# Kernel optimization log

Hardware: AMD Instinct MI355X
Metric: run time of the kernel (lower is better)

## Reference

```python
import jax, jax.numpy as jnp
import numpy as np

B, C, H, W = 512, 64, 32, 64
NUM_NODE = 128


def setup_inputs() -> dict:
    key = jax.random.key(0)
    ks = jax.random.split(key, 11)
    f = jnp.float32
    def nrm(k, shape, s):
        return jax.random.normal(k, shape, f) * s
    return {
        "x":   jax.random.normal(ks[0], (B, C, H, W), f),
        "w11": nrm(ks[1], (32, 64, 1, 1), 0.1), "b11": nrm(ks[2], (32,), 0.05),
        "w12": nrm(ks[3], (16, 32, 3, 3), 0.1), "b12": nrm(ks[4], (16,), 0.05),
        "w21": nrm(ks[5], (8, 16, 1, 1), 0.1),  "b21": nrm(ks[6], (8,), 0.05),
        "w22": nrm(ks[7], (4, 8, 3, 3), 0.1),   "b22": nrm(ks[8], (4,), 0.05),
        "fcw": nrm(ks[9], (2 * NUM_NODE, 32 * 64 * 4), 0.05),
        "fcb": nrm(ks[10], (2 * NUM_NODE,), 0.05),
    }


def _conv_relu(x, w, b, pad):
    y = jax.lax.conv_general_dilated(
        x, w, window_strides=(1, 1), padding=[(pad, pad), (pad, pad)],
        dimension_numbers=("NCHW", "OIHW", "NCHW"))
    return jax.nn.relu(y + b[None, :, None, None])


def reference(x, w11, b11, w12, b12, w21, b21, w22, b22, fcw, fcb):
    # --- GraphGen3: conv stack -> fc -> n_Sigmoid -> [B, N, 2] ---
    h = _conv_relu(x, w11, b11, 0)
    h = _conv_relu(h, w12, b12, 1)
    h = _conv_relu(h, w21, b21, 0)
    h = _conv_relu(h, w22, b22, 1)          # [B, 4, 32, 64]
    z = h.reshape(h.shape[0], -1) @ fcw.T + fcb  # [B, 2N]
    c01 = jax.nn.sigmoid(3.0 * z).reshape(x.shape[0], -1, 2)  # n_Sigmoid(x, 3)
    # --- get_coord: scale normalized coords to pixel range ---
    Hd, Wd = x.shape[2], x.shape[3]
    coord = c01 * jnp.array([Hd - 1, Wd - 1], x.dtype)  # [B, N, 2]
    # --- th_batch_map_coordinates: clamp, corner gather, bilinear lerp ---
    ch = jnp.clip(coord[..., 0], 0.0, Hd - 1)
    cw = jnp.clip(coord[..., 1], 0.0, Wd - 1)
    h0 = jnp.floor(ch).astype(jnp.int32); h1 = jnp.ceil(ch).astype(jnp.int32)
    w0 = jnp.floor(cw).astype(jnp.int32); w1 = jnp.ceil(cw).astype(jnp.int32)
    bidx = jnp.arange(x.shape[0])[:, None]  # [B, 1]
    def gv(hi, wi):
        return x[bidx, :, hi, wi]           # gather -> [B, N, C]
    v_lt = gv(h0, w0); v_rt = gv(h1, w0)
    v_lb = gv(h0, w1); v_rb = gv(h1, w1)
    oh = (ch - h0.astype(x.dtype))[..., None]
    ow = (cw - w0.astype(x.dtype))[..., None]
    vt = v_lt + oh * (v_rt - v_lt)
    vb = v_lb + oh * (v_rb - v_lb)
    graph_feat = vt + ow * (vb - vt)        # [B, N, C] (matches permute(0,2,1))
    return graph_feat, coord
```

## Files before the change

### kernel.cpp

```cpp
#include <hip/hip_runtime.h>
#include <hip/hip_fp16.h>
#include <cstdint>

#define BATCH 512
#define CIN   64
#define HH    32
#define WW    64
#define HW    2048
#define C1    32
#define C2    16
#define C3    8
#define C4    4
#define NOUT  256
#define KFC   8192
#define NODES 128
#define KS    16
#define GF_SIZE (BATCH * NODES * CIN)

typedef __attribute__((ext_vector_type(8))) short bfrag;
typedef __attribute__((ext_vector_type(4))) float ffrag;

__device__ __forceinline__ ushort bf_trunc(float f) { return (ushort)(__float_as_uint(f) >> 16); }
__device__ __forceinline__ float  bf_truncf(float f) { return __uint_as_float(__float_as_uint(f) & 0xffff0000u); }
__device__ __forceinline__ ushort f2bf(float f) {
  uint32_t u = __float_as_uint(f);
  return (ushort)((u + 0x7fffu + ((u >> 16) & 1u)) >> 16);
}
__device__ __forceinline__ uint32_t pack2(float a, float b) {
  return (uint32_t)f2bf(a) | ((uint32_t)f2bf(b) << 16);
}
__device__ __forceinline__ uint32_t packhi2(float a, float b) {
  return (uint32_t)bf_trunc(a) | ((uint32_t)bf_trunc(b) << 16);
}
__device__ __forceinline__ ushort f2h(float f) { return __half_as_ushort(__float2half_rn(f)); }
__device__ __forceinline__ uint32_t packh2(float a, float b) {
  return (uint32_t)f2h(a) | ((uint32_t)f2h(b) << 16);
}
__device__ __forceinline__ float h2f(uint32_t u) { return __half2float(__ushort_as_half((ushort)u)); }
__device__ __forceinline__ float bf2f(ushort u) { return __uint_as_float(((uint32_t)u) << 16); }

__device__ __forceinline__ bfrag ld_frag4(const uint32_t* tp) {
  union { uint32_t u[4]; bfrag b; } c;
  c.u[0] = tp[0]; c.u[1] = tp[1]; c.u[2] = tp[2]; c.u[3] = tp[3];
  return c.b;
}

__global__ __launch_bounds__(256) void k_front(
    const float* __restrict__ x, const float* __restrict__ w11, const float* __restrict__ b11,
    const float* __restrict__ fcw, ushort* __restrict__ fcwh, ushort* __restrict__ fcwl,
    ushort* __restrict__ xt, ushort* __restrict__ h1g)
{
  if (blockIdx.y >= BATCH) {
    const int chunk = (blockIdx.y - BATCH) * 8 + blockIdx.x;
    const int i = (chunk * 256 + threadIdx.x) * 8;
    const float4 a = *(const float4*)(fcw + i);
    const float4 b = *(const float4*)(fcw + i + 4);
    uint4 hv, lv;
    hv.x = packhi2(a.x, a.y); hv.y = packhi2(a.z, a.w);
    hv.z = packhi2(b.x, b.y); hv.w = packhi2(b.z, b.w);
    lv.x = pack2(a.x - bf_truncf(a.x), a.y - bf_truncf(a.y));
    lv.y = pack2(a.z - bf_truncf(a.z), a.w - bf_truncf(a.w));
    lv.z = pack2(b.x - bf_truncf(b.x), b.y - bf_truncf(b.y));
    lv.w = pack2(b.z - bf_truncf(b.z), b.w - bf_truncf(b.w));
    *(uint4*)(fcwh + i) = hv;
    *(uint4*)(fcwl + i) = lv;
    return;
  }

  __shared__ uint32_t tb[256 * 33];
  const int t  = threadIdx.x;
  const int b  = blockIdx.y;
  const int rg = blockIdx.x;
  {
    const float* xp = x + (size_t)b * CIN * HW + rg * 256 + t;
    #pragma unroll
    for (int j = 0; j < 32; ++j) {
      float v0 = xp[(size_t)(2 * j) * HW];
      float v1 = xp[(size_t)(2 * j + 1) * HW];
      tb[t * 33 + j] = pack2(v0, v1);
    }
  }
  __syncthreads();

  {
    ushort* op = xt + ((size_t)b * HW + rg * 256) * CIN;
    #pragma unroll
    for (int k = 0; k < 8; ++k) {
      const int u = k * 256 + t;
      const int p = u >> 3, q = u & 7;
      uint4 v;
      v.x = tb[p * 33 + q * 4 + 0];
      v.y = tb[p * 33 + q * 4 + 1];
      v.z = tb[p * 33 + q * 4 + 2];
      v.w = tb[p * 33 + q * 4 + 3];
      *(uint4*)(op + (size_t)u * 8) = v;
    }
  }

  const int l  = t & 63;
  const int wv = t >> 6;
  const int lr = l & 15;
  const int lg = l >> 4;
  bfrag w1h[2][2], w1l[2][2];
  #pragma unroll
  for (int m = 0; m < 2; ++m) {
    #pragma unroll
    for (int ks = 0; ks < 2; ++ks) {
      const float* wp = w11 + (m * 16 + lr) * 64 + ks * 32 + lg * 8;
      #pragma unroll
      for (int e = 0; e < 8; ++e) {
        float v = wp[e];
        w1h[m][ks][e] = (short)bf_trunc(v);
        w1l[m][ks][e] = (short)f2bf(v - bf_truncf(v));
      }
    }
  }
  float bias1[2][4];
  #pragma unroll
  for (int m = 0; m < 2; ++m) {
    #pragma unroll
    for (int r = 0; r < 4; ++r) bias1[m][r] = b11[m * 16 + lg * 4 + r];
  }

  #pragma unroll
  for (int i = 0; i < 4; ++i) {
    const int pxl = (wv * 4 + i) * 16 + lr;
    const bfrag f0 = ld_frag4(&tb[pxl * 33 + lg * 4]);
    const bfrag f1 = ld_frag4(&tb[pxl * 33 + 16 + lg * 4]);
    ffrag a0 = {0.f, 0.f, 0.f, 0.f}, a1 = {0.f, 0.f, 0.f, 0.f};
    a0 = __builtin_amdgcn_mfma_f32_16x16x32_bf16(w1h[0][0], f0, a0, 0, 0, 0);
    a0 = __builtin_amdgcn_mfma_f32_16x16x32_bf16(w1l[0][0], f0, a0, 0, 0, 0);
    a0 = __builtin_amdgcn_mfma_f32_16x16x32_bf16(w1h[0][1], f1, a0, 0, 0, 0);
    a0 = __builtin_amdgcn_mfma_f32_16x16x32_bf16(w1l[0][1], f1, a0, 0, 0, 0);
    a1 = __builtin_amdgcn_mfma_f32_16x16x32_bf16(w1h[1][0], f0, a1, 0, 0, 0);
    a1 = __builtin_amdgcn_mfma_f32_16x16x32_bf16(w1l[1][0], f0, a1, 0, 0, 0);
    a1 = __builtin_amdgcn_mfma_f32_16x16x32_bf16(w1h[1][1], f1, a1, 0, 0, 0);
    a1 = __builtin_amdgcn_mfma_f32_16x16x32_bf16(w1l[1][1], f1, a1, 0, 0, 0);
    ushort* hp = h1g + ((size_t)b * HW + rg * 256 + pxl) * C1;
    #pragma unroll
    for (int m = 0; m < 2; ++m) {
      float v0 = fmaxf((m ? a1[0] : a0[0]) + bias1[m][0], 0.f);
      float v1 = fmaxf((m ? a1[1] : a0[1]) + bias1[m][1], 0.f);
      float v2 = fmaxf((m ? a1[2] : a0[2]) + bias1[m][2], 0.f);
      float v3 = fmaxf((m ? a1[3] : a0[3]) + bias1[m][3], 0.f);
      *(uint2*)(hp + m * 16 + lg * 4) = uint2{pack2(v0, v1), pack2(v2, v3)};
    }
  }
}

__global__ __launch_bounds__(256) void k_conv234(
    const ushort* __restrict__ h1g, const float* __restrict__ w12, const float* __restrict__ b12,
    const float* __restrict__ w21, const float* __restrict__ b21,
    const float* __restrict__ w22, const float* __restrict__ b22,
    ushort* __restrict__ h4, int b0)
{
  __shared__ __align__(16) char smem[12 * 66 * 64];
  const int tid = threadIdx.x;
  const int l   = tid & 63;
  const int wv  = tid >> 6;
  const int lr  = l & 15;
  const int lg  = l >> 4;
  const int r0  = blockIdx.x * 8;
  const int bg  = b0 + blockIdx.y;

  if (tid < 192) {
    int row = tid >> 4, half = (tid >> 3) & 1, q = tid & 7;
    int cell = row * 66 + (half ? 65 : 0);
    *(uint2*)(smem + (cell << 6) + q * 8) = uint2{0u, 0u};
  }

  {
    const int px = tid >> 2, q = tid & 3;
    const int colb  = px + 1;
    const int chunk = q ^ ((colb >> 1) & 3);
    #pragma unroll
    for (int ry = 0; ry < 12; ++ry) {
      const int y = r0 - 2 + ry;
      uint4 v = uint4{0u, 0u, 0u, 0u};
      if (y >= 0 && y < HH)
        v = *(const uint4*)(h1g + ((size_t)bg * HW + y * WW + px) * C1 + q * 8);
      *(uint4*)(smem + ((ry * 66 + colb) << 6) + (chunk << 4)) = v;
    }
  }
  __syncthreads();

  bfrag w2h[9], w2l[9];
  #pragma unroll
  for (int t = 0; t < 9; ++t) {
    const float* wp = w12 + lr * 288 + t;
    #pragma unroll
    for (int e = 0; e < 8; ++e) {
      float v = wp[(lg * 8 + e) * 9];
      w2h[t][e] = (short)bf_trunc(v);
      w2l[t][e] = (short)f2bf(v - bf_truncf(v));
    }
  }
  float bias2[4];
  #pragma unroll
  for (int r = 0; r < 4; ++r) bias2[r] = b12[lg * 4 + r];

  uint32_t ph0[10], ph1[10];
  #pragma unroll
  for (int i = 0; i < 10; ++i) {
    const int nt   = wv * 10 + i;
    const int hryo = nt >> 2;
    const int col0 = (nt & 3) << 4;
    ffrag acc = {0.f, 0.f, 0.f, 0.f};
    #pragma unroll
    for (int ky = 0; ky < 3; ++ky) {
      const int row = hryo + ky;
      #pragma unroll
      for (int kx = 0; kx < 3; ++kx) {
        const int colb  = col0 + lr + kx;
        const int chunk = lg ^ ((colb >> 1) & 3);
        const bfrag hv = *(const bfrag*)(smem + ((row * 66 + colb) << 6) + (chunk << 4));
        acc = __builtin_amdgcn_mfma_f32_16x16x32_bf16(w2h[ky * 3 + kx], hv, acc, 0, 0, 0);
        acc = __builtin_amdgcn_mfma_f32_16x16x32_bf16(w2l[ky * 3 + kx], hv, acc, 0, 0, 0);
      }
    }
    ph0[i] = packh2(fmaxf(acc[0] + bias2[0], 0.f), fmaxf(acc[1] + bias2[1], 0.f));
    ph1[i] = packh2(fmaxf(acc[2] + bias2[2], 0.f), fmaxf(acc[3] + bias2[3], 0.f));
  }
  __syncthreads();

  #pragma unroll
  for (int i = 0; i < 10; ++i) {
    const int nt   = wv * 10 + i;
    const int hryo = nt >> 2;
    const int col  = ((nt & 3) << 4) + lr;
    *(uint2*)(smem + ((hryo * 64 + col) << 5) + lg * 8) = uint2{ph0[i], ph1[i]};
  }
  __syncthreads();

  float* h3b = (float*)(smem + 20480);
  for (int p = tid; p < 640; p += 256) {
    const int ry = p >> 6, wc = p & 63;
    const int y  = r0 - 1 + ry;
    float* hd = h3b + (ry * 64 + wc) * 9;
    if (y >= 0 && y < HH) {
      const uint4 ua = *(const uint4*)(smem + ((ry * 64 + wc) << 5));
      const uint4 ub = *(const uint4*)(smem + ((ry * 64 + wc) << 5) + 16);
      uint32_t uw[8] = {ua.x, ua.y, ua.z, ua.w, ub.x, ub.y, ub.z, ub.w};
      float xv[16];
      #pragma unroll
      for (int j = 0; j < 8; ++j) {
        xv[2*j]   = h2f(uw[j] & 0xffffu);
        xv[2*j+1] = h2f(uw[j] >> 16);
      }
      float acc[C3];
      #pragma unroll
      for (int o = 0; o < C3; ++o) acc[o] = b21[o];
      #pragma unroll
      for (int c = 0; c < 16; ++c) {
        float v = xv[c];
        #pragma unroll
        for (int o = 0; o < C3; ++o)
          acc[o] = fmaf(v, w21[o * 16 + c], acc[o]);
      }
      #pragma unroll
      for (int c = 0; c < C3; ++c) hd[c] = fmaxf(acc[c], 0.f);
    } else {
      #pragma unroll
      for (int c = 0; c < C3; ++c) hd[c] = 0.f;
    }
  }
  __syncthreads();

  for (int p = tid; p < 512; p += 256) {
    const int yl = p >> 6, wc = p & 63, ry = yl + 1;
    float acc[C4] = {b22[0], b22[1], b22[2], b22[3]};
    #pragma unroll
    for (int ky = 0; ky < 3; ++ky) {
      #pragma unroll
      for (int kx = 0; kx < 3; ++kx) {
        const int wcc = wc + kx - 1;
        if (wcc < 0 || wcc >= WW) continue;
        const float* hb = h3b + ((ry + ky - 1) * 64 + wcc) * 9;
        const int tap = ky * 3 + kx;
        #pragma unroll
        for (int c = 0; c < C3; ++c) {
          float v = hb[c];
          #pragma unroll
          for (int o = 0; o < C4; ++o)
            acc[o] = fmaf(v, w22[(o * 8 + c) * 9 + tap], acc[o]);
        }
      }
    }
    const size_t base = (size_t)blockIdx.y * KFC + (r0 + yl) * WW + wc;
    #pragma unroll
    for (int o = 0; o < C4; ++o)
      h4[base + (size_t)o * HW] = f2bf(fmaxf(acc[o], 0.f));
  }
}

__global__ __launch_bounds__(256) void k_fc(
    const ushort* __restrict__ Ap_, const ushort* __restrict__ Bhp,
    const ushort* __restrict__ Blp, float* __restrict__ zpart, int cb)
{
  const int tid = threadIdx.x;
  const int l   = tid & 63;
  const int wv  = tid >> 6;
  const int lr  = l & 15;
  const int lg  = l >> 4;
  const int m0  = blockIdx.x * 64 + (wv >> 1) * 32;
  const int n0  = blockIdx.y * 64 + (wv & 1) * 32;
  const int k0  = blockIdx.z * (KFC / KS);

  int mrow[2], nrow[2];
  #pragma unroll
  for (int t = 0; t < 2; ++t) {
    int m = m0 + t * 16 + lr;
    mrow[t] = m < cb ? m : cb - 1;
    nrow[t] = n0 + t * 16 + lr;
  }
  ffrag acc[2][2] = {};

  #pragma unroll 1
  for (int kc = 0; kc < (KFC / KS) / 32; ++kc) {
    const int k = k0 + kc * 32 + lg * 8;
    bfrag ah[2], bh[2], bl[2];
    #pragma unroll
    for (int t = 0; t < 2; ++t) {
      ah[t] = *(const bfrag*)(Ap_ + (size_t)mrow[t] * KFC + k);
      bh[t] = *(const bfrag*)(Bhp + (size_t)nrow[t] * KFC + k);
      bl[t] = *(const bfrag*)(Blp + (size_t)nrow[t] * KFC + k);
    }
    #pragma unroll
    for (int mt = 0; mt < 2; ++mt) {
      #pragma unroll
      for (int nt = 0; nt < 2; ++nt) {
        acc[mt][nt] = __builtin_amdgcn_mfma_f32_16x16x32_bf16(ah[mt], bh[nt], acc[mt][nt], 0, 0, 0);
        acc[mt][nt] = __builtin_amdgcn_mfma_f32_16x16x32_bf16(ah[mt], bl[nt], acc[mt][nt], 0, 0, 0);
      }
    }
  }

  #pragma unroll
  for (int mt = 0; mt < 2; ++mt) {
    #pragma unroll
    for (int r = 0; r < 4; ++r) {
      const int m = m0 + mt * 16 + lg * 4 + r;
      if (m < cb) {
        #pragma unroll
        for (int nt = 0; nt < 2; ++nt)
          zpart[((size_t)blockIdx.z * cb + m) * NOUT + n0 + nt * 16 + lr] = acc[mt][nt][r];
      }
    }
  }
}

__global__ __launch_bounds__(256) void k_gather(
    const ushort* __restrict__ xt, const float* __restrict__ zpart,
    const float* __restrict__ fcb, float* __restrict__ out, int cb, int b0)
{
  const int bid = blockIdx.x;
  int bl, g;
  if ((cb & 7) == 0) {
    const int xcd = bid & 7;
    const int j   = bid >> 3;
    g  = j & 31;
    bl = (j >> 5) * 8 + xcd;
  } else {
    bl = bid >> 5;
    g  = bid & 31;
  }
  const int node = g * 4 + (threadIdx.x >> 6);
  const int l    = threadIdx.x & 63;
  const int bg   = b0 + bl;

  float val = 0.f;
  if (l < 2 * KS) {
    const int kb = l >> 1, comp = l & 1;
    val = zpart[((size_t)kb * cb + bl) * NOUT + node * 2 + comp];
  }
  #pragma unroll
  for (int off = 2; off < 2 * KS; off <<= 1) val += __shfl_xor(val, off);
  const float z0 = __shfl(val, 0) + fcb[node * 2 + 0];
  const float z1 = __shfl(val, 1) + fcb[node * 2 + 1];
  const float ch = 31.f / (1.f + __expf(-3.f * z0));
  const float cw = 63.f / (1.f + __expf(-3.f * z1));

  if (l < 2)
    out[GF_SIZE + (((size_t)bg * NODES + node) << 1) + l] = l ? cw : ch;

  const float chv = fminf(fmaxf(ch, 0.f), 31.f);
  const float cwv = fminf(fmaxf(cw, 0.f), 63.f);
  const float fh = floorf(chv), fw = floorf(cwv);
  const int h0 = (int)fh, h1i = (int)ceilf(chv);
  const int w0 = (int)fw, w1i = (int)ceilf(cwv);
  const float oh = chv - fh, ow = cwv - fw;
  const ushort* xbp = xt + (size_t)bg * HW * CIN + l;
  const float v_lt = bf2f(xbp[(size_t)(h0 * WW + w0) * CIN]);
  const float v_rt = bf2f(xbp[(size_t)(h1i * WW + w0) * CIN]);
  const float v_lb = bf2f(xbp[(size_t)(h0 * WW + w1i) * CIN]);
  const float v_rb = bf2f(xbp[(size_t)(h1i * WW + w1i) * CIN]);
  const float vt = v_lt + oh * (v_rt - v_lt);
  const float vb = v_lb + oh * (v_rb - v_lb);
  out[((size_t)bg * NODES + node) * CIN + l] = vt + ow * (vb - vt);
}

extern "C" void kernel_launch(void* const* d_in, const int* in_sizes, int n_in,
                              void* d_out, int out_size, void* d_ws, size_t ws_size,
                              hipStream_t stream)
{
  (void)in_sizes; (void)n_in; (void)out_size;
  const float* x   = (const float*)d_in[0];
  const float* w11 = (const float*)d_in[1];
  const float* b11 = (const float*)d_in[2];
  const float* w12 = (const float*)d_in[3];
  const float* b12 = (const float*)d_in[4];
  const float* w21 = (const float*)d_in[5];
  const float* b21 = (const float*)d_in[6];
  const float* w22 = (const float*)d_in[7];
  const float* b22 = (const float*)d_in[8];
  const float* fcw = (const float*)d_in[9];
  const float* fcb = (const float*)d_in[10];
  float* out = (float*)d_out;
  char* wsb  = (char*)d_ws;

  const size_t xtBytes = (size_t)BATCH * HW * CIN * 2;
  const size_t h1Bytes = (size_t)BATCH * HW * C1 * 2;
  const size_t perB    = 16384 + (size_t)KS * NOUT * 4;
  const size_t fixed   = xtBytes + h1Bytes + 2 * 4194304;
  size_t avail = ws_size > fixed ? ws_size - fixed : perB;
  size_t cbmax = avail / perB;
  int CB = (int)(cbmax < (size_t)BATCH ? cbmax : (size_t)BATCH);
  if (CB < 1) CB = 1;

  char* p = wsb;
  ushort* xtv  = (ushort*)p;  p += xtBytes;
  ushort* h1v  = (ushort*)p;  p += h1Bytes;
  ushort* h4v  = (ushort*)p;  p += (size_t)CB * 16384;
  float*  zpv  = (float*)p;   p += (size_t)CB * KS * NOUT * 4;
  ushort* fcwh = (ushort*)p;  p += 4194304;
  ushort* fcwl = (ushort*)p;

  k_front<<<dim3(8, BATCH + 128), 256, 0, stream>>>(x, w11, b11, fcw, fcwh, fcwl,
                                                    xtv, h1v);

  for (int b0 = 0; b0 < BATCH; b0 += CB) {
    const int cb = (BATCH - b0 < CB) ? (BATCH - b0) : CB;
    k_conv234<<<dim3(4, cb), 256, 0, stream>>>(h1v, w12, b12, w21, b21, w22, b22,
                                               h4v, b0);
    k_fc<<<dim3((cb + 63) / 64, 4, KS), 256, 0, stream>>>(h4v, fcwh, fcwl, zpv, cb);
    k_gather<<<dim3(cb * 32), 256, 0, stream>>>(xtv, zpv, fcb, out, cb, b0);
  }
}
```

Before: 212.6 us.

## Fuse all stages into one persistent cooperative kernel with grid syncs

Replaces the four separate launches (front, conv234, fc, gather) with a single persistent cooperative kernel that loops over tiles for each stage and separates stages with grid-wide syncs. The goal is to remove launch overhead and inter-kernel gaps. It also drops workspace-based batch chunking and assumes the workspace holds the full batch. In exchange, the persistent grid is limited by occupancy of a large fused kernel with 50KB shared memory, which may lower parallelism per stage, and grid syncs add their own cost.

```diff
diff --git a/kernel.cpp b/kernel.cpp
--- a/kernel.cpp
+++ b/kernel.cpp
@@ -1,6 +1,9 @@
 #include <hip/hip_runtime.h>
 #include <hip/hip_fp16.h>
+#include <hip/hip_cooperative_groups.h>
 #include <cstdint>
+
+namespace cg = cooperative_groups;
 
 #define BATCH 512
 #define CIN   64
@@ -43,6 +46,327 @@
   union { uint32_t u[4]; bfrag b; } c;
   c.u[0] = tp[0]; c.u[1] = tp[1]; c.u[2] = tp[2]; c.u[3] = tp[3];
   return c.b;
+}
+
+__global__ __launch_bounds__(256) void k_mega(
+    const float* __restrict__ x, const float* __restrict__ w11, const float* __restrict__ b11,
+    const float* __restrict__ w12, const float* __restrict__ b12,
+    const float* __restrict__ w21, const float* __restrict__ b21,
+    const float* __restrict__ w22, const float* __restrict__ b22,
+    const float* __restrict__ fcw, const float* __restrict__ fcb,
+    ushort* __restrict__ fcwh, ushort* __restrict__ fcwl,
+    ushort* __restrict__ xt, ushort* __restrict__ h1g, ushort* __restrict__ h4,
+    float* __restrict__ zpart, float* __restrict__ out)
+{
+  __shared__ __align__(16) char smem[50688];
+  cg::grid_group gg = cg::this_grid();
+  const int tid = threadIdx.x;
+  const int l   = tid & 63;
+  const int wv  = tid >> 6;
+  const int lr  = l & 15;
+  const int lg  = l >> 4;
+
+  {
+    bfrag w1h[2][2], w1l[2][2];
+    #pragma unroll
+    for (int m = 0; m < 2; ++m)
+      #pragma unroll
+      for (int ks = 0; ks < 2; ++ks) {
+        const float* wp = w11 + (m * 16 + lr) * 64 + ks * 32 + lg * 8;
+        #pragma unroll
+        for (int e = 0; e < 8; ++e) {
+          float v = wp[e];
+          w1h[m][ks][e] = (short)bf_trunc(v);
+          w1l[m][ks][e] = (short)f2bf(v - bf_truncf(v));
+        }
+      }
+    float bias1[2][4];
+    #pragma unroll
+    for (int m = 0; m < 2; ++m)
+      #pragma unroll
+      for (int r = 0; r < 4; ++r) bias1[m][r] = b11[m * 16 + lg * 4 + r];
+
+    uint32_t* tb = (uint32_t*)smem;
+    for (int tile = blockIdx.x; tile < 5120; tile += gridDim.x) {
+      if (tile >= 4096) {
+        const int chunk = tile - 4096;
+        const int i = (chunk * 256 + tid) * 8;
+        const float4 a = *(const float4*)(fcw + i);
+        const float4 b = *(const float4*)(fcw + i + 4);
+        uint4 hv, lv;
+        hv.x = packhi2(a.x, a.y); hv.y = packhi2(a.z, a.w);
+        hv.z = packhi2(b.x, b.y); hv.w = packhi2(b.z, b.w);
+        lv.x = pack2(a.x - bf_truncf(a.x), a.y - bf_truncf(a.y));
+        lv.y = pack2(a.z - bf_truncf(a.z), a.w - bf_truncf(a.w));
+        lv.z = pack2(b.x - bf_truncf(b.x), b.y - bf_truncf(b.y));
+        lv.w = pack2(b.z - bf_truncf(b.z), b.w - bf_truncf(b.w));
+        *(uint4*)(fcwh + i) = hv;
+        *(uint4*)(fcwl + i) = lv;
+        continue;
+      }
+      const int b  = tile >> 3;
+      const int rg = tile & 7;
+      {
+        const float* xp = x + (size_t)b * CIN * HW + rg * 256 + tid;
+        #pragma unroll
+        for (int j = 0; j < 32; ++j) {
+          float v0 = xp[(size_t)(2 * j) * HW];
+          float v1 = xp[(size_t)(2 * j + 1) * HW];
+          tb[tid * 33 + j] = pack2(v0, v1);
+        }
+      }
+      __syncthreads();
+      {
+        ushort* op = xt + ((size_t)b * HW + rg * 256) * CIN;
+        #pragma unroll
+        for (int k = 0; k < 8; ++k) {
+          const int u = k * 256 + tid;
+          const int p = u >> 3, q = u & 7;
+          uint4 v;
+          v.x = tb[p * 33 + q * 4 + 0];
+          v.y = tb[p * 33 + q * 4 + 1];
+          v.z = tb[p * 33 + q * 4 + 2];
+          v.w = tb[p * 33 + q * 4 + 3];
+          *(uint4*)(op + (size_t)u * 8) = v;
+        }
+      }
+      #pragma unroll
+      for (int i = 0; i < 4; ++i) {
+        const int pxl = (wv * 4 + i) * 16 + lr;
+        const bfrag f0 = ld_frag4(&tb[pxl * 33 + lg * 4]);
+        const bfrag f1 = ld_frag4(&tb[pxl * 33 + 16 + lg * 4]);
+        ffrag a0 = {0.f, 0.f, 0.f, 0.f}, a1 = {0.f, 0.f, 0.f, 0.f};
+        a0 = __builtin_amdgcn_mfma_f32_16x16x32_bf16(w1h[0][0], f0, a0, 0, 0, 0);
+        a0 = __builtin_amdgcn_mfma_f32_16x16x32_bf16(w1l[0][0], f0, a0, 0, 0, 0);
+        a0 = __builtin_amdgcn_mfma_f32_16x16x32_bf16(w1h[0][1], f1, a0, 0, 0, 0);
+        a0 = __builtin_amdgcn_mfma_f32_16x16x32_bf16(w1l[0][1], f1, a0, 0, 0, 0);
+        a1 = __builtin_amdgcn_mfma_f32_16x16x32_bf16(w1h[1][0], f0, a1, 0, 0, 0);
+        a1 = __builtin_amdgcn_mfma_f32_16x16x32_bf16(w1l[1][0], f0, a1, 0, 0, 0);
+        a1 = __builtin_amdgcn_mfma_f32_16x16x32_bf16(w1h[1][1], f1, a1, 0, 0, 0);
+        a1 = __builtin_amdgcn_mfma_f32_16x16x32_bf16(w1l[1][1], f1, a1, 0, 0, 0);
+        ushort* hp = h1g + ((size_t)b * HW + rg * 256 + pxl) * C1;
+        #pragma unroll
+        for (int m = 0; m < 2; ++m) {
+          float v0 = fmaxf((m ? a1[0] : a0[0]) + bias1[m][0], 0.f);
+          float v1 = fmaxf((m ? a1[1] : a0[1]) + bias1[m][1], 0.f);
+          float v2 = fmaxf((m ? a1[2] : a0[2]) + bias1[m][2], 0.f);
+          float v3 = fmaxf((m ? a1[3] : a0[3]) + bias1[m][3], 0.f);
+          *(uint2*)(hp + m * 16 + lg * 4) = uint2{pack2(v0, v1), pack2(v2, v3)};
+        }
+      }
+      __syncthreads();
+    }
+  }
+  gg.sync();
+
+  for (int tile = blockIdx.x; tile < 2048; tile += gridDim.x) {
+    const int bg = tile >> 2;
+    const int r0 = (tile & 3) * 8;
+
+    if (tid < 192) {
+      int row = tid >> 4, half = (tid >> 3) & 1, q = tid & 7;
+      int cell = row * 66 + (half ? 65 : 0);
+      *(uint2*)(smem + (cell << 6) + q * 8) = uint2{0u, 0u};
+    }
+    {
+      const int px = tid >> 2, q = tid & 3;
+      const int colb  = px + 1;
+      const int chunk = q ^ ((colb >> 1) & 3);
+      #pragma unroll
+      for (int ry = 0; ry < 12; ++ry) {
+        const int y = r0 - 2 + ry;
+        uint4 v = uint4{0u, 0u, 0u, 0u};
+        if (y >= 0 && y < HH)
+          v = *(const uint4*)(h1g + ((size_t)bg * HW + y * WW + px) * C1 + q * 8);
+        *(uint4*)(smem + ((ry * 66 + colb) << 6) + (chunk << 4)) = v;
+      }
+    }
+    __syncthreads();
+
+    bfrag w2h[9], w2l[9];
+    #pragma unroll
+    for (int t = 0; t < 9; ++t) {
+      const float* wp = w12 + lr * 288 + t;
+      #pragma unroll
+      for (int e = 0; e < 8; ++e) {
+        float v = wp[(lg * 8 + e) * 9];
+        w2h[t][e] = (short)bf_trunc(v);
+        w2l[t][e] = (short)f2bf(v - bf_truncf(v));
+      }
+    }
+    float bias2[4];
+    #pragma unroll
+    for (int r = 0; r < 4; ++r) bias2[r] = b12[lg * 4 + r];
+
+    uint32_t ph0[10], ph1[10];
+    #pragma unroll
+    for (int i = 0; i < 10; ++i) {
+      const int nt   = wv * 10 + i;
+      const int hryo = nt >> 2;
+      const int col0 = (nt & 3) << 4;
+      ffrag acc = {0.f, 0.f, 0.f, 0.f};
+      #pragma unroll
+      for (int ky = 0; ky < 3; ++ky) {
+        const int row = hryo + ky;
+        #pragma unroll
+        for (int kx = 0; kx < 3; ++kx) {
+          const int colb  = col0 + lr + kx;
+          const int chunk = lg ^ ((colb >> 1) & 3);
+          const bfrag hv = *(const bfrag*)(smem + ((row * 66 + colb) << 6) + (chunk << 4));
+          acc = __builtin_amdgcn_mfma_f32_16x16x32_bf16(w2h[ky * 3 + kx], hv, acc, 0, 0, 0);
+          acc = __builtin_amdgcn_mfma_f32_16x16x32_bf16(w2l[ky * 3 + kx], hv, acc, 0, 0, 0);
+        }
+      }
+      ph0[i] = packh2(fmaxf(acc[0] + bias2[0], 0.f), fmaxf(acc[1] + bias2[1], 0.f));
+      ph1[i] = packh2(fmaxf(acc[2] + bias2[2], 0.f), fmaxf(acc[3] + bias2[3], 0.f));
+    }
+    __syncthreads();
+
+    #pragma unroll
+    for (int i = 0; i < 10; ++i) {
+      const int nt   = wv * 10 + i;
+      const int hryo = nt >> 2;
+      const int col  = ((nt & 3) << 4) + lr;
+      *(uint2*)(smem + ((hryo * 64 + col) << 5) + lg * 8) = uint2{ph0[i], ph1[i]};
+    }
+    __syncthreads();
+
+    float* h3b = (float*)(smem + 20480);
+    for (int p = tid; p < 640; p += 256) {
+      const int ry = p >> 6, wc = p & 63;
+      const int y  = r0 - 1 + ry;
+      float* hd = h3b + (ry * 64 + wc) * 9;
+      if (y >= 0 && y < HH) {
+        const uint4 ua = *(const uint4*)(smem + ((ry * 64 + wc) << 5));
+        const uint4 ub = *(const uint4*)(smem + ((ry * 64 + wc) << 5) + 16);
+        uint32_t uw[8] = {ua.x, ua.y, ua.z, ua.w, ub.x, ub.y, ub.z, ub.w};
+        float xv[16];
+        #pragma unroll
+        for (int j = 0; j < 8; ++j) {
+          xv[2*j]   = h2f(uw[j] & 0xffffu);
+          xv[2*j+1] = h2f(uw[j] >> 16);
+        }
+        float acc[C3];
+        #pragma unroll
+        for (int o = 0; o < C3; ++o) acc[o] = b21[o];
+        #pragma unroll
+        for (int c = 0; c < 16; ++c) {
+          float v = xv[c];
+          #pragma unroll
+          for (int o = 0; o < C3; ++o)
+            acc[o] = fmaf(v, w21[o * 16 + c], acc[o]);
+        }
+        #pragma unroll
+        for (int c = 0; c < C3; ++c) hd[c] = fmaxf(acc[c], 0.f);
+      } else {
+        #pragma unroll
+        for (int c = 0; c < C3; ++c) hd[c] = 0.f;
+      }
+    }
+    __syncthreads();
+
+    for (int p = tid; p < 512; p += 256) {
+      const int yl = p >> 6, wc = p & 63, ry = yl + 1;
+      float acc[C4] = {b22[0], b22[1], b22[2], b22[3]};
+      #pragma unroll
+      for (int ky = 0; ky < 3; ++ky) {
+        #pragma unroll
+        for (int kx = 0; kx < 3; ++kx) {
+          const int wcc = wc + kx - 1;
+          if (wcc < 0 || wcc >= WW) continue;
+          const float* hb = h3b + ((ry + ky - 1) * 64 + wcc) * 9;
+          const int tap = ky * 3 + kx;
+          #pragma unroll
+          for (int c = 0; c < C3; ++c) {
+            float v = hb[c];
+            #pragma unroll
+            for (int o = 0; o < C4; ++o)
+              acc[o] = fmaf(v, w22[(o * 8 + c) * 9 + tap], acc[o]);
+          }
+        }
+      }
+      const size_t base = (size_t)bg * KFC + (r0 + yl) * WW + wc;
+      #pragma unroll
+      for (int o = 0; o < C4; ++o)
+        h4[base + (size_t)o * HW] = f2bf(fmaxf(acc[o], 0.f));
+    }
+    __syncthreads();
+  }
+  gg.sync();
+
+  for (int tile = blockIdx.x; tile < 512; tile += gridDim.x) {
+    const int mb = tile & 7, nb = (tile >> 3) & 3, kb = tile >> 5;
+    const int m0 = mb * 64 + (wv >> 1) * 32;
+    const int n0 = nb * 64 + (wv & 1) * 32;
+    const int k0 = kb * (KFC / KS);
+    ffrag acc[2][2] = {};
+    #pragma unroll 1
+    for (int kc = 0; kc < (KFC / KS) / 32; ++kc) {
+      const int k = k0 + kc * 32 + lg * 8;
+      bfrag ah[2], bh[2], bl[2];
+      #pragma unroll
+      for (int t = 0; t < 2; ++t) {
+        ah[t] = *(const bfrag*)(h4 + (size_t)(m0 + t * 16 + lr) * KFC + k);
+        bh[t] = *(const bfrag*)(fcwh + (size_t)(n0 + t * 16 + lr) * KFC + k);
+        bl[t] = *(const bfrag*)(fcwl + (size_t)(n0 + t * 16 + lr) * KFC + k);
+      }
+      #pragma unroll
+      for (int mt = 0; mt < 2; ++mt)
+        #pragma unroll
+        for (int nt = 0; nt < 2; ++nt) {
+          acc[mt][nt] = __builtin_amdgcn_mfma_f32_16x16x32_bf16(ah[mt], bh[nt], acc[mt][nt], 0, 0, 0);
+          acc[mt][nt] = __builtin_amdgcn_mfma_f32_16x16x32_bf16(ah[mt], bl[nt], acc[mt][nt], 0, 0, 0);
+        }
+    }
+    #pragma unroll
+    for (int mt = 0; mt < 2; ++mt)
+      #pragma unroll
+      for (int r = 0; r < 4; ++r) {
+        const int m = m0 + mt * 16 + lg * 4 + r;
+        #pragma unroll
+        for (int nt = 0; nt < 2; ++nt)
+          zpart[((size_t)kb * BATCH + m) * NOUT + n0 + nt * 16 + lr] = acc[mt][nt][r];
+      }
+  }
+  gg.sync();
+
+  for (int tile = blockIdx.x; tile < 16384; tile += gridDim.x) {
+    const int xcd = tile & 7;
+    const int j   = tile >> 3;
+    const int g   = j & 31;
+    const int bg  = (j >> 5) * 8 + xcd;
+    const int node = g * 4 + (tid >> 6);
+
+    float val = 0.f;
+    if (l < 2 * KS) {
+      const int kb = l >> 1, comp = l & 1;
+      val = zpart[((size_t)kb * BATCH + bg) * NOUT + node * 2 + comp];
+    }
+    #pragma unroll
+    for (int off = 2; off < 2 * KS; off <<= 1) val += __shfl_xor(val, off);
+    const float z0 = __shfl(val, 0) + fcb[node * 2 + 0];
+    const float z1 = __shfl(val, 1) + fcb[node * 2 + 1];
+    const float ch = 31.f / (1.f + __expf(-3.f * z0));
+    const float cw = 63.f / (1.f + __expf(-3.f * z1));
+
+    if (l < 2)
+      out[GF_SIZE + (((size_t)bg * NODES + node) << 1) + l] = l ? cw : ch;
+
+    const float chv = fminf(fmaxf(ch, 0.f), 31.f);
+    const float cwv = fminf(fmaxf(cw, 0.f), 63.f);
+    const float fh = floorf(chv), fw = floorf(cwv);
+    const int h0 = (int)fh, h1i = (int)ceilf(chv);
+    const int w0 = (int)fw, w1i = (int)ceilf(cwv);
+    const float oh = chv - fh, ow = cwv - fw;
+    const ushort* xbp = xt + (size_t)bg * HW * CIN + l;
+    const float v_lt = bf2f(xbp[(size_t)(h0 * WW + w0) * CIN]);
+    const float v_rt = bf2f(xbp[(size_t)(h1i * WW + w0) * CIN]);
+    const float v_lb = bf2f(xbp[(size_t)(h0 * WW + w1i) * CIN]);
+    const float v_rb = bf2f(xbp[(size_t)(h1i * WW + w1i) * CIN]);
+    const float vt = v_lt + oh * (v_rt - v_lt);
+    const float vb = v_lb + oh * (v_rb - v_lb);
+    out[((size_t)bg * NODES + node) * CIN + l] = vt + ow * (vb - vt);
+  }
 }
 
 __global__ __launch_bounds__(256) void k_front(
@@ -66,7 +390,6 @@
     *(uint4*)(fcwl + i) = lv;
     return;
   }
-
   __shared__ uint32_t tb[256 * 33];
   const int t  = threadIdx.x;
   const int b  = blockIdx.y;
@@ -81,7 +404,6 @@
     }
   }
   __syncthreads();
-
   {
     ushort* op = xt + ((size_t)b * HW + rg * 256) * CIN;
     #pragma unroll
@@ -96,14 +418,13 @@
       *(uint4*)(op + (size_t)u * 8) = v;
     }
   }
-
   const int l  = t & 63;
   const int wv = t >> 6;
   const int lr = l & 15;
   const int lg = l >> 4;
   bfrag w1h[2][2], w1l[2][2];
   #pragma unroll
-  for (int m = 0; m < 2; ++m) {
+  for (int m = 0; m < 2; ++m)
     #pragma unroll
     for (int ks = 0; ks < 2; ++ks) {
       const float* wp = w11 + (m * 16 + lr) * 64 + ks * 32 + lg * 8;
@@ -114,13 +435,11 @@
         w1l[m][ks][e] = (short)f2bf(v - bf_truncf(v));
       }
     }
-  }
   float bias1[2][4];
   #pragma unroll
-  for (int m = 0; m < 2; ++m) {
+  for (int m = 0; m < 2; ++m)
     #pragma unroll
     for (int r = 0; r < 4; ++r) bias1[m][r] = b11[m * 16 + lg * 4 + r];
-  }
 
   #pragma unroll
   for (int i = 0; i < 4; ++i) {
@@ -168,7 +487,6 @@
     int cell = row * 66 + (half ? 65 : 0);
     *(uint2*)(smem + (cell << 6) + q * 8) = uint2{0u, 0u};
   }
-
   {
     const int px = tid >> 2, q = tid & 3;
     const int colb  = px + 1;
@@ -222,7 +540,6 @@
     ph1[i] = packh2(fmaxf(acc[2] + bias2[2], 0.f), fmaxf(acc[3] + bias2[3], 0.f));
   }
   __syncthreads();
-
   #pragma unroll
   for (int i = 0; i < 10; ++i) {
     const int nt   = wv * 10 + i;
@@ -305,48 +622,36 @@
   const int m0  = blockIdx.x * 64 + (wv >> 1) * 32;
   const int n0  = blockIdx.y * 64 + (wv & 1) * 32;
   const int k0  = blockIdx.z * (KFC / KS);
-
-  int mrow[2], nrow[2];
-  #pragma unroll
-  for (int t = 0; t < 2; ++t) {
-    int m = m0 + t * 16 + lr;
-    mrow[t] = m < cb ? m : cb - 1;
-    nrow[t] = n0 + t * 16 + lr;
-  }
   ffrag acc[2][2] = {};
-
   #pragma unroll 1
   for (int kc = 0; kc < (KFC / KS) / 32; ++kc) {
     const int k = k0 + kc * 32 + lg * 8;
     bfrag ah[2], bh[2], bl[2];
     #pragma unroll
     for (int t = 0; t < 2; ++t) {
-      ah[t] = *(const bfrag*)(Ap_ + (size_t)mrow[t] * KFC + k);
-      bh[t] = *(const bfrag*)(Bhp + (size_t)nrow[t] * KFC + k);
-      bl[t] = *(const bfrag*)(Blp + (size_t)nrow[t] * KFC + k);
-    }
-    #pragma unroll
-    for (int mt = 0; mt < 2; ++mt) {
+      int m = m0 + t * 16 + lr; if (m >= cb) m = cb - 1;
+      ah[t] = *(const bfrag*)(Ap_ + (size_t)m * KFC + k);
+      bh[t] = *(const bfrag*)(Bhp + (size_t)(n0 + t * 16 + lr) * KFC + k);
+      bl[t] = *(const bfrag*)(Blp + (size_t)(n0 + t * 16 + lr) * KFC + k);
+    }
+    #pragma unroll
+    for (int mt = 0; mt < 2; ++mt)
       #pragma unroll
       for (int nt = 0; nt < 2; ++nt) {
         acc[mt][nt] = __builtin_amdgcn_mfma_f32_16x16x32_bf16(ah[mt], bh[nt], acc[mt][nt], 0, 0, 0);
         acc[mt][nt] = __builtin_amdgcn_mfma_f32_16x16x32_bf16(ah[mt], bl[nt], acc[mt][nt], 0, 0, 0);
       }
-    }
-  }
-
-  #pragma unroll
-  for (int mt = 0; mt < 2; ++mt) {
+  }
+  #pragma unroll
+  for (int mt = 0; mt < 2; ++mt)
     #pragma unroll
     for (int r = 0; r < 4; ++r) {
       const int m = m0 + mt * 16 + lg * 4 + r;
-      if (m < cb) {
+      if (m < cb)
         #pragma unroll
         for (int nt = 0; nt < 2; ++nt)
           zpart[((size_t)blockIdx.z * cb + m) * NOUT + n0 + nt * 16 + lr] = acc[mt][nt][r];
-      }
-    }
-  }
+    }
 }
 
 __global__ __launch_bounds__(256) void k_gather(
@@ -367,7 +672,6 @@
   const int node = g * 4 + (threadIdx.x >> 6);
   const int l    = threadIdx.x & 63;
   const int bg   = b0 + bl;
-
   float val = 0.f;
   if (l < 2 * KS) {
     const int kb = l >> 1, comp = l & 1;
@@ -379,10 +683,8 @@
   const float z1 = __shfl(val, 1) + fcb[node * 2 + 1];
   const float ch = 31.f / (1.f + __expf(-3.f * z0));
   const float cw = 63.f / (1.f + __expf(-3.f * z1));
-
   if (l < 2)
     out[GF_SIZE + (((size_t)bg * NODES + node) << 1) + l] = l ? cw : ch;
-
   const float chv = fminf(fmaxf(ch, 0.f), 31.f);
   const float cwv = fminf(fmaxf(cw, 0.f), 63.f);
   const float fh = floorf(chv), fw = floorf(cwv);
@@ -403,7 +705,7 @@
                               void* d_out, int out_size, void* d_ws, size_t ws_size,
                               hipStream_t stream)
 {
-  (void)in_sizes; (void)n_in; (void)out_size;
+  (void)in_sizes; (void)n_in; (void)out_size; (void)ws_size;
   const float* x   = (const float*)d_in[0];
   const float* w11 = (const float*)d_in[1];
   const float* b11 = (const float*)d_in[2];
@@ -416,33 +718,41 @@
   const float* fcw = (const float*)d_in[9];
   const float* fcb = (const float*)d_in[10];
   float* out = (float*)d_out;
-  char* wsb  = (char*)d_ws;
-
-  const size_t xtBytes = (size_t)BATCH * HW * CIN * 2;
-  const size_t h1Bytes = (size_t)BATCH * HW * C1 * 2;
-  const size_t perB    = 16384 + (size_t)KS * NOUT * 4;
-  const size_t fixed   = xtBytes + h1Bytes + 2 * 4194304;
-  size_t avail = ws_size > fixed ? ws_size - fixed : perB;
-  size_t cbmax = avail / perB;
-  int CB = (int)(cbmax < (size_t)BATCH ? cbmax : (size_t)BATCH);
-  if (CB < 1) CB = 1;
-
-  char* p = wsb;
-  ushort* xtv  = (ushort*)p;  p += xtBytes;
-  ushort* h1v  = (ushort*)p;  p += h1Bytes;
-  ushort* h4v  = (ushort*)p;  p += (size_t)CB * 16384;
-  float*  zpv  = (float*)p;   p += (size_t)CB * KS * NOUT * 4;
-  ushort* fcwh = (ushort*)p;  p += 4194304;
+  char* p = (char*)d_ws;
+
+  ushort* xtv  = (ushort*)p;  p += (size_t)BATCH * HW * CIN * 2;
+  ushort* h1v  = (ushort*)p;  p += (size_t)BATCH * HW * C1 * 2;
+  ushort* h4v  = (ushort*)p;  p += (size_t)BATCH * KFC * 2;
+  float*  zpv  = (float*)p;   p += (size_t)KS * BATCH * NOUT * 4;
+  ushort* fcwh = (ushort*)p;  p += (size_t)NOUT * KFC * 2;
   ushort* fcwl = (ushort*)p;
 
-  k_front<<<dim3(8, BATCH + 128), 256, 0, stream>>>(x, w11, b11, fcw, fcwh, fcwl,
-                                                    xtv, h1v);
-
-  for (int b0 = 0; b0 < BATCH; b0 += CB) {
-    const int cb = (BATCH - b0 < CB) ? (BATCH - b0) : CB;
-    k_conv234<<<dim3(4, cb), 256, 0, stream>>>(h1v, w12, b12, w21, b21, w22, b22,
-                                               h4v, b0);
-    k_fc<<<dim3((cb + 63) / 64, 4, KS), 256, 0, stream>>>(h4v, fcwh, fcwl, zpv, cb);
-    k_gather<<<dim3(cb * 32), 256, 0, stream>>>(xtv, zpv, fcb, out, cb, b0);
-  }
-}
+  int dev = 0;
+  hipGetDevice(&dev);
+  hipDeviceProp_t prop;
+  hipError_t e1 = hipGetDeviceProperties(&prop, dev);
+  int maxb = 0;
+  hipError_t e2 = hipOccupancyMaxActiveBlocksPerMultiprocessor(&maxb, (const void*)k_mega, 256, 0);
+  const bool coop = (e1 == hipSuccess) && (e2 == hipSuccess) &&
+                    prop.cooperativeLaunch && maxb >= 1;
+
+  if (coop) {
+    int nblk = maxb * prop.multiProcessorCount;
+    if (nblk < 1) nblk = 1;
+    void* args[] = {
+      (void*)&x, (void*)&w11, (void*)&b11, (void*)&w12, (void*)&b12,
+      (void*)&w21, (void*)&b21, (void*)&w22, (void*)&b22,
+      (void*)&fcw, (void*)&fcb,
+      (void*)&fcwh, (void*)&fcwl, (void*)&xtv, (void*)&h1v, (void*)&h4v,
+      (void*)&zpv, (void*)&out };
+    hipLaunchCooperativeKernel((const void*)k_mega, dim3(nblk), dim3(256),
+                               args, 0, stream);
+  } else {
+    k_front<<<dim3(8, BATCH + 128), 256, 0, stream>>>(x, w11, b11, fcw, fcwh, fcwl,
+                                                      xtv, h1v);
+    k_conv234<<<dim3(4, BATCH), 256, 0, stream>>>(h1v, w12, b12, w21, b21, w22, b22,
+                                                  h4v, 0);
+    k_fc<<<dim3(BATCH / 64, 4, KS), 256, 0, stream>>>(h4v, fcwh, fcwl, zpv, BATCH);
+    k_gather<<<dim3(BATCH * 32), 256, 0, stream>>>(xtv, zpv, fcb, out, BATCH, 0);
+  }
+}
```

New measurement: 212.9 us. Within noise of the previous version (+0.1%).

## Drop bf16 transposed x copy; gather from fp32 x and launch full batch

Applied to the files above, without the earlier changes.

k_front no longer writes a channels-last bf16 copy of x (64 MB of stores). k_gather now reads the four bilinear corners straight from the original fp32 NCHW input. That makes the gathered values exact, but the per-channel reads are strided by HW instead of contiguous. The host-side batch-chunking loop is also gone: one launch of each kernel covers all 512 batch items, on the assumption that the workspace is large enough.

```diff
diff --git a/kernel.cpp b/kernel.cpp
--- a/kernel.cpp
+++ b/kernel.cpp
@@ -37,7 +37,6 @@
   return (uint32_t)f2h(a) | ((uint32_t)f2h(b) << 16);
 }
 __device__ __forceinline__ float h2f(uint32_t u) { return __half2float(__ushort_as_half((ushort)u)); }
-__device__ __forceinline__ float bf2f(ushort u) { return __uint_as_float(((uint32_t)u) << 16); }
 
 __device__ __forceinline__ bfrag ld_frag4(const uint32_t* tp) {
   union { uint32_t u[4]; bfrag b; } c;
@@ -48,7 +47,7 @@
 __global__ __launch_bounds__(256) void k_front(
     const float* __restrict__ x, const float* __restrict__ w11, const float* __restrict__ b11,
     const float* __restrict__ fcw, ushort* __restrict__ fcwh, ushort* __restrict__ fcwl,
-    ushort* __restrict__ xt, ushort* __restrict__ h1g)
+    ushort* __restrict__ h1g)
 {
   if (blockIdx.y >= BATCH) {
     const int chunk = (blockIdx.y - BATCH) * 8 + blockIdx.x;
@@ -82,28 +81,13 @@
   }
   __syncthreads();
 
-  {
-    ushort* op = xt + ((size_t)b * HW + rg * 256) * CIN;
-    #pragma unroll
-    for (int k = 0; k < 8; ++k) {
-      const int u = k * 256 + t;
-      const int p = u >> 3, q = u & 7;
-      uint4 v;
-      v.x = tb[p * 33 + q * 4 + 0];
-      v.y = tb[p * 33 + q * 4 + 1];
-      v.z = tb[p * 33 + q * 4 + 2];
-      v.w = tb[p * 33 + q * 4 + 3];
-      *(uint4*)(op + (size_t)u * 8) = v;
-    }
-  }
-
   const int l  = t & 63;
   const int wv = t >> 6;
   const int lr = l & 15;
   const int lg = l >> 4;
   bfrag w1h[2][2], w1l[2][2];
   #pragma unroll
-  for (int m = 0; m < 2; ++m) {
+  for (int m = 0; m < 2; ++m)
     #pragma unroll
     for (int ks = 0; ks < 2; ++ks) {
       const float* wp = w11 + (m * 16 + lr) * 64 + ks * 32 + lg * 8;
@@ -114,13 +98,11 @@
         w1l[m][ks][e] = (short)f2bf(v - bf_truncf(v));
       }
     }
-  }
   float bias1[2][4];
   #pragma unroll
-  for (int m = 0; m < 2; ++m) {
+  for (int m = 0; m < 2; ++m)
     #pragma unroll
     for (int r = 0; r < 4; ++r) bias1[m][r] = b11[m * 16 + lg * 4 + r];
-  }
 
   #pragma unroll
   for (int i = 0; i < 4; ++i) {
@@ -168,7 +150,6 @@
     int cell = row * 66 + (half ? 65 : 0);
     *(uint2*)(smem + (cell << 6) + q * 8) = uint2{0u, 0u};
   }
-
   {
     const int px = tid >> 2, q = tid & 3;
     const int colb  = px + 1;
@@ -222,7 +203,6 @@
     ph1[i] = packh2(fmaxf(acc[2] + bias2[2], 0.f), fmaxf(acc[3] + bias2[3], 0.f));
   }
   __syncthreads();
-
   #pragma unroll
   for (int i = 0; i < 10; ++i) {
     const int nt   = wv * 10 + i;
@@ -305,52 +285,40 @@
   const int m0  = blockIdx.x * 64 + (wv >> 1) * 32;
   const int n0  = blockIdx.y * 64 + (wv & 1) * 32;
   const int k0  = blockIdx.z * (KFC / KS);
-
-  int mrow[2], nrow[2];
-  #pragma unroll
-  for (int t = 0; t < 2; ++t) {
-    int m = m0 + t * 16 + lr;
-    mrow[t] = m < cb ? m : cb - 1;
-    nrow[t] = n0 + t * 16 + lr;
-  }
   ffrag acc[2][2] = {};
-
   #pragma unroll 1
   for (int kc = 0; kc < (KFC / KS) / 32; ++kc) {
     const int k = k0 + kc * 32 + lg * 8;
     bfrag ah[2], bh[2], bl[2];
     #pragma unroll
     for (int t = 0; t < 2; ++t) {
-      ah[t] = *(const bfrag*)(Ap_ + (size_t)mrow[t] * KFC + k);
-      bh[t] = *(const bfrag*)(Bhp + (size_t)nrow[t] * KFC + k);
-      bl[t] = *(const bfrag*)(Blp + (size_t)nrow[t] * KFC + k);
-    }
-    #pragma unroll
-    for (int mt = 0; mt < 2; ++mt) {
+      int m = m0 + t * 16 + lr; if (m >= cb) m = cb - 1;
+      ah[t] = *(const bfrag*)(Ap_ + (size_t)m * KFC + k);
+      bh[t] = *(const bfrag*)(Bhp + (size_t)(n0 + t * 16 + lr) * KFC + k);
+      bl[t] = *(const bfrag*)(Blp + (size_t)(n0 + t * 16 + lr) * KFC + k);
+    }
+    #pragma unroll
+    for (int mt = 0; mt < 2; ++mt)
       #pragma unroll
       for (int nt = 0; nt < 2; ++nt) {
         acc[mt][nt] = __builtin_amdgcn_mfma_f32_16x16x32_bf16(ah[mt], bh[nt], acc[mt][nt], 0, 0, 0);
         acc[mt][nt] = __builtin_amdgcn_mfma_f32_16x16x32_bf16(ah[mt], bl[nt], acc[mt][nt], 0, 0, 0);
       }
-    }
-  }
-
-  #pragma unroll
-  for (int mt = 0; mt < 2; ++mt) {
+  }
+  #pragma unroll
+  for (int mt = 0; mt < 2; ++mt)
     #pragma unroll
     for (int r = 0; r < 4; ++r) {
       const int m = m0 + mt * 16 + lg * 4 + r;
-      if (m < cb) {
+      if (m < cb)
         #pragma unroll
         for (int nt = 0; nt < 2; ++nt)
           zpart[((size_t)blockIdx.z * cb + m) * NOUT + n0 + nt * 16 + lr] = acc[mt][nt][r];
-      }
-    }
-  }
+    }
 }
 
 __global__ __launch_bounds__(256) void k_gather(
-    const ushort* __restrict__ xt, const float* __restrict__ zpart,
+    const float* __restrict__ x, const float* __restrict__ zpart,
     const float* __restrict__ fcb, float* __restrict__ out, int cb, int b0)
 {
   const int bid = blockIdx.x;
@@ -389,11 +357,11 @@
   const int h0 = (int)fh, h1i = (int)ceilf(chv);
   const int w0 = (int)fw, w1i = (int)ceilf(cwv);
   const float oh = chv - fh, ow = cwv - fw;
-  const ushort* xbp = xt + (size_t)bg * HW * CIN + l;
-  const float v_lt = bf2f(xbp[(size_t)(h0 * WW + w0) * CIN]);
-  const float v_rt = bf2f(xbp[(size_t)(h1i * WW + w0) * CIN]);
-  const float v_lb = bf2f(xbp[(size_t)(h0 * WW + w1i) * CIN]);
-  const float v_rb = bf2f(xbp[(size_t)(h1i * WW + w1i) * CIN]);
+  const float* xbp = x + ((size_t)bg * CIN + l) * HW;
+  const float v_lt = xbp[h0 * WW + w0];
+  const float v_rt = xbp[h1i * WW + w0];
+  const float v_lb = xbp[h0 * WW + w1i];
+  const float v_rb = xbp[h1i * WW + w1i];
   const float vt = v_lt + oh * (v_rt - v_lt);
   const float vb = v_lb + oh * (v_rb - v_lb);
   out[((size_t)bg * NODES + node) * CIN + l] = vt + ow * (vb - vt);
@@ -403,7 +371,7 @@
                               void* d_out, int out_size, void* d_ws, size_t ws_size,
                               hipStream_t stream)
 {
-  (void)in_sizes; (void)n_in; (void)out_size;
+  (void)in_sizes; (void)n_in; (void)out_size; (void)ws_size;
   const float* x   = (const float*)d_in[0];
   const float* w11 = (const float*)d_in[1];
   const float* b11 = (const float*)d_in[2];
@@ -416,33 +384,16 @@
   const float* fcw = (const float*)d_in[9];
   const float* fcb = (const float*)d_in[10];
   float* out = (float*)d_out;
-  char* wsb  = (char*)d_ws;
-
-  const size_t xtBytes = (size_t)BATCH * HW * CIN * 2;
-  const size_t h1Bytes = (size_t)BATCH * HW * C1 * 2;
-  const size_t perB    = 16384 + (size_t)KS * NOUT * 4;
-  const size_t fixed   = xtBytes + h1Bytes + 2 * 4194304;
-  size_t avail = ws_size > fixed ? ws_size - fixed : perB;
-  size_t cbmax = avail / perB;
-  int CB = (int)(cbmax < (size_t)BATCH ? cbmax : (size_t)BATCH);
-  if (CB < 1) CB = 1;
-
-  char* p = wsb;
-  ushort* xtv  = (ushort*)p;  p += xtBytes;
-  ushort* h1v  = (ushort*)p;  p += h1Bytes;
-  ushort* h4v  = (ushort*)p;  p += (size_t)CB * 16384;
-  float*  zpv  = (float*)p;   p += (size_t)CB * KS * NOUT * 4;
-  ushort* fcwh = (ushort*)p;  p += 4194304;
+  char* p = (char*)d_ws;
+
+  ushort* h1v  = (ushort*)p;  p += (size_t)BATCH * HW * C1 * 2;
+  ushort* h4v  = (ushort*)p;  p += (size_t)BATCH * KFC * 2;
+  float*  zpv  = (float*)p;   p += (size_t)KS * BATCH * NOUT * 4;
+  ushort* fcwh = (ushort*)p;  p += (size_t)NOUT * KFC * 2;
   ushort* fcwl = (ushort*)p;
 
-  k_front<<<dim3(8, BATCH + 128), 256, 0, stream>>>(x, w11, b11, fcw, fcwh, fcwl,
-                                                    xtv, h1v);
-
-  for (int b0 = 0; b0 < BATCH; b0 += CB) {
-    const int cb = (BATCH - b0 < CB) ? (BATCH - b0) : CB;
-    k_conv234<<<dim3(4, cb), 256, 0, stream>>>(h1v, w12, b12, w21, b21, w22, b22,
-                                               h4v, b0);
-    k_fc<<<dim3((cb + 63) / 64, 4, KS), 256, 0, stream>>>(h4v, fcwh, fcwl, zpv, cb);
-    k_gather<<<dim3(cb * 32), 256, 0, stream>>>(xtv, zpv, fcb, out, cb, b0);
-  }
-}
+  k_front<<<dim3(8, BATCH + 128), 256, 0, stream>>>(x, w11, b11, fcw, fcwh, fcwl, h1v);
+  k_conv234<<<dim3(4, BATCH), 256, 0, stream>>>(h1v, w12, b12, w21, b21, w22, b22, h4v, 0);
+  k_fc<<<dim3(BATCH / 64, 4, KS), 256, 0, stream>>>(h4v, fcwh, fcwl, zpv, BATCH);
+  k_gather<<<dim3(BATCH * 32), 256, 0, stream>>>(x, zpv, fcb, out, BATCH, 0);
+}
```

New measurement: 242.7 us. +14.1%, slower.
